# Kernel tuning notes

Hardware: AMD Instinct MI355X
Metric: run time of the kernel (lower is better)

## Reference

```python
import jax, jax.numpy as jnp
import numpy as np

IMG = (3, 64, 64)
CHANNELS = 256
PRIM_DIM = 8
NUM_CLASSES = 50
OUT_DIM = 16
NUM_ROUTING = 3
K = 9
IN_CAPS = (CHANNELS // PRIM_DIM) * 24 * 24  # 18432
DN = ('NCHW', 'OIHW', 'NCHW')


def squash(v, axis=-1):
    sn = jnp.sum(v * v, axis=axis, keepdims=True)
    return sn / (1.0 + sn) * v / (jnp.sqrt(sn) + 1e-8)


def setup_inputs() -> dict:
    key = jax.random.key(0)
    ks = jax.random.split(key, 12)
    s = 0.01
    return {
        'x': jax.random.normal(ks[0], (8,) + IMG, jnp.float32),
        'conv1_w': s * jax.random.normal(ks[1], (CHANNELS, 3, K, K), jnp.float32),
        'conv1_b': jnp.zeros((CHANNELS,), jnp.float32),
        'prim_w': s * jax.random.normal(ks[2], (CHANNELS, CHANNELS, K, K), jnp.float32),
        'prim_b': jnp.zeros((CHANNELS,), jnp.float32),
        'W': s * jax.random.normal(ks[3], (NUM_CLASSES, IN_CAPS, OUT_DIM, PRIM_DIM), jnp.float32),
        'd1_w': s * jax.random.normal(ks[4], (512, OUT_DIM * NUM_CLASSES), jnp.float32),
        'd1_b': jnp.zeros((512,), jnp.float32),
        'd2_w': s * jax.random.normal(ks[5], (1024, 512), jnp.float32),
        'd2_b': jnp.zeros((1024,), jnp.float32),
        'd3_w': s * jax.random.normal(ks[6], (int(np.prod(IMG)), 1024), jnp.float32),
        'd3_b': jnp.zeros((int(np.prod(IMG)),), jnp.float32),
    }


def reference(x, conv1_w, conv1_b, prim_w, prim_b, W, d1_w, d1_b, d2_w, d2_b, d3_w, d3_b):
    B = x.shape[0]
    # conv1 + relu: [B,3,64,64] -> [B,256,56,56]
    h = jax.lax.conv_general_dilated(x, conv1_w, (1, 1), 'VALID', dimension_numbers=DN)
    h = jax.nn.relu(h + conv1_b[None, :, None, None])
    # primary capsules: [B,256,24,24] -> [B,18432,8]
    p = jax.lax.conv_general_dilated(h, prim_w, (2, 2), 'VALID', dimension_numbers=DN)
    p = p + prim_b[None, :, None, None]
    p = p.reshape(B, CHANNELS // PRIM_DIM, p.shape[2], p.shape[3], PRIM_DIM)
    u = squash(p.reshape(B, -1, PRIM_DIM))
    # predictions u_hat: [B, num_caps, in_caps, out_dim]
    u_hat = jnp.einsum('nide,bie->bnid', W, u)
    temp = jax.lax.stop_gradient(u_hat)
    b_log = jnp.zeros((B, NUM_CLASSES, IN_CAPS, 1), jnp.float32)
    for _ in range(NUM_ROUTING - 1):
        sc = jax.nn.softmax(b_log, axis=1)
        v = squash(jnp.sum(sc * temp, axis=2))            # [B,nc,dc]
        b_log = b_log + jnp.einsum('bnid,bnd->bni', temp, v)[..., None]
    sc = jax.nn.softmax(b_log, axis=1)
    v = squash(jnp.sum(sc * u_hat, axis=2))               # [B,nc,dc]
    preds = jnp.linalg.norm(v, axis=-1)                   # [B,nc]
    idx = jnp.argmax(preds, axis=1)
    y = jax.nn.one_hot(idx, NUM_CLASSES, dtype=v.dtype)[..., None]
    r = (v * y).reshape(B, -1)
    r = jax.nn.relu(r @ d1_w.T + d1_b)
    r = jax.nn.relu(r @ d2_w.T + d2_b)
    r = jax.nn.sigmoid(r @ d3_w.T + d3_b)
    recon = r.reshape(B, *IMG)
    return preds, recon
```

## Files before the change

### kernel.cpp

```cpp
#include <hip/hip_runtime.h>

typedef short short8 __attribute__((ext_vector_type(8)));
typedef float f32x4 __attribute__((ext_vector_type(4)));
typedef _Float16 h2 __attribute__((ext_vector_type(2)));

__device__ __forceinline__ unsigned short f2bf(float f) {
  union { float f; unsigned u; } a; a.f = f;
  unsigned r = a.u + 0x7fffu + ((a.u >> 16) & 1u);
  return (unsigned short)(r >> 16);
}

__device__ __forceinline__ h2 u2h2(unsigned w) {
  union { unsigned u; h2 h; } q; q.u = w; return q.h;
}

#if __has_builtin(__builtin_amdgcn_fdot2)
#define FDOT2(a, b, c) __builtin_amdgcn_fdot2((a), (b), (c), false)
#else
#define FDOT2(a, b, c) ((c) + (float)(a)[0] * (float)(b)[0] + (float)(a)[1] * (float)(b)[1])
#endif

__global__ void offtab_k(unsigned* __restrict__ off_tab) {
  const int k = blockIdx.x * 256 + threadIdx.x;
  const int ci = k / 81, rr = k % 81;
  const int ky = rr / 9, kx = rr % 9;
  off_tab[k] = (unsigned)(ci * 3136 + ky * 56 + kx);
}

__global__ __launch_bounds__(256) void wconv_k(const float* __restrict__ pw,
                                               unsigned short* __restrict__ wbf) {
  const int kb = blockIdx.x, co = threadIdx.x;
  const float4* src = (const float4*)(pw + (long)co * 20736 + kb * 8);
  const float4 a = src[0], b = src[1];
  union { unsigned short s[8]; short8 v; } o;
  o.s[0] = f2bf(a.x); o.s[1] = f2bf(a.y); o.s[2] = f2bf(a.z); o.s[3] = f2bf(a.w);
  o.s[4] = f2bf(b.x); o.s[5] = f2bf(b.y); o.s[6] = f2bf(b.z); o.s[7] = f2bf(b.w);
  *reinterpret_cast<short8*>(&wbf[((long)kb * 256 + co) * 8]) = o.v;
}

__global__ __launch_bounds__(256) void conv1_k(const float* __restrict__ x,
                                               const float* __restrict__ w,
                                               const float* __restrict__ bias,
                                               unsigned short* __restrict__ h_bf) {
  __shared__ float xl[12288];
  __shared__ float wl[244];
  const int blk = blockIdx.x;
  const int b = blk >> 8, co = blk & 255;
  const int t = threadIdx.x;
  const float4* xb = (const float4*)(x + b * 12288);
  float4* xl4 = (float4*)xl;
  for (int r = t; r < 3072; r += 256) xl4[r] = xb[r];
  for (int r = t; r < 243; r += 256) wl[r] = w[co * 243 + r];
  __syncthreads();
  if (t >= 224) return;
  const int ox = t % 56, oy0 = (t / 56) * 14;
  float acc[14];
#pragma unroll
  for (int j = 0; j < 14; ++j) acc[j] = 0.f;
  for (int ci = 0; ci < 3; ++ci)
    for (int kx = 0; kx < 9; ++kx) {
      const int base = ci * 4096 + oy0 * 64 + ox + kx;
      float win[22];
#pragma unroll
      for (int q = 0; q < 22; ++q) win[q] = xl[base + q * 64];
#pragma unroll
      for (int ky = 0; ky < 9; ++ky) {
        const float wv = wl[ci * 81 + ky * 9 + kx];
#pragma unroll
        for (int j = 0; j < 14; ++j) acc[j] = fmaf(wv, win[j + ky], acc[j]);
      }
    }
  const float bv = bias[co];
  unsigned short* hp = h_bf + (((long)b * 256 + co) * 56 + oy0) * 56 + ox;
#pragma unroll
  for (int j = 0; j < 14; ++j) {
    float v = acc[j] + bv;
    v = v > 0.f ? v : 0.f;
    hp[j * 56] = f2bf(v);
  }
}

__global__ __launch_bounds__(512) void prim_gemm(const unsigned short* __restrict__ h_bf,
                                                 const uint4* __restrict__ wbf4,
                                                 const unsigned* __restrict__ off_tab,
                                                 float* __restrict__ C_part) {
  __shared__ uint4 A4[256];
  __shared__ uint4 B4[1024];
  const int t = threadIdx.x;
  const int lane = t & 63, w = t >> 6;
  const int mt = blockIdx.x, kz = blockIdx.y;
  const int k0 = kz * 5184;
  const bool isA = (t < 256);
  const int ar = t & 63, ac = (t >> 6) & 3;
  const int m = mt * 64 + ar;
  const int b = m / 576, yx = m % 576;
  const int oy = yx / 24, ox = yx % 24;
  const long base_p = (long)b * 802816 + oy * 112 + ox * 2;
  const int bco = t & 255;
  const int wm = w >> 2, wn = w & 3;
  const int fr = lane & 15, fg = lane >> 4;
  f32x4 acc[2][4];
#pragma unroll
  for (int i2 = 0; i2 < 2; ++i2)
#pragma unroll
    for (int j = 0; j < 4; ++j)
#pragma unroll
      for (int e = 0; e < 4; ++e) acc[i2][j][e] = 0.f;

  union { unsigned short s[8]; uint4 v; } pa;
  uint4 pb0, pb1, pb2, pb3;
  auto loadA = [&](int kt) {
    const int kb = k0 + kt * 32 + ac * 8;
#pragma unroll
    for (int j = 0; j < 8; ++j) pa.s[j] = h_bf[base_p + off_tab[kb + j]];
  };
  auto loadB = [&](int kt) {
    const int kb0 = (k0 + kt * 32) >> 3;
    pb0 = wbf4[(kb0 + 0) * 256 + bco];
    pb1 = wbf4[(kb0 + 1) * 256 + bco];
    pb2 = wbf4[(kb0 + 2) * 256 + bco];
    pb3 = wbf4[(kb0 + 3) * 256 + bco];
  };
  if (isA) loadA(0); else loadB(0);

  const short8* A8 = (const short8*)A4;
  const short8* B8 = (const short8*)B4;
  for (int kt = 0; kt < 162; ++kt) {
    __syncthreads();
    if (isA) {
      A4[ac * 64 + ar] = pa.v;
    } else {
      B4[bco] = pb0;
      B4[256 + bco] = pb1;
      B4[512 + bco] = pb2;
      B4[768 + bco] = pb3;
    }
    if (kt < 161) { if (isA) loadA(kt + 1); else loadB(kt + 1); }
    __syncthreads();
    const short8 a0 = A8[fg * 64 + wm * 32 + fr];
    const short8 a1 = A8[fg * 64 + wm * 32 + 16 + fr];
    const short8 b0 = B8[fg * 256 + wn * 64 + fr];
    const short8 b1 = B8[fg * 256 + wn * 64 + 16 + fr];
    const short8 b2 = B8[fg * 256 + wn * 64 + 32 + fr];
    const short8 b3 = B8[fg * 256 + wn * 64 + 48 + fr];
    acc[0][0] = __builtin_amdgcn_mfma_f32_16x16x32_bf16(a0, b0, acc[0][0], 0, 0, 0);
    acc[0][1] = __builtin_amdgcn_mfma_f32_16x16x32_bf16(a0, b1, acc[0][1], 0, 0, 0);
    acc[0][2] = __builtin_amdgcn_mfma_f32_16x16x32_bf16(a0, b2, acc[0][2], 0, 0, 0);
    acc[0][3] = __builtin_amdgcn_mfma_f32_16x16x32_bf16(a0, b3, acc[0][3], 0, 0, 0);
    acc[1][0] = __builtin_amdgcn_mfma_f32_16x16x32_bf16(a1, b0, acc[1][0], 0, 0, 0);
    acc[1][1] = __builtin_amdgcn_mfma_f32_16x16x32_bf16(a1, b1, acc[1][1], 0, 0, 0);
    acc[1][2] = __builtin_amdgcn_mfma_f32_16x16x32_bf16(a1, b2, acc[1][2], 0, 0, 0);
    acc[1][3] = __builtin_amdgcn_mfma_f32_16x16x32_bf16(a1, b3, acc[1][3], 0, 0, 0);
  }
#pragma unroll
  for (int i2 = 0; i2 < 2; ++i2)
#pragma unroll
    for (int j = 0; j < 4; ++j)
#pragma unroll
      for (int e = 0; e < 4; ++e) {
        const int row = mt * 64 + wm * 32 + i2 * 16 + fg * 4 + e;
        const int col = wn * 64 + j * 16 + fr;
        C_part[((long)kz * 4608 + row) * 256 + col] = acc[i2][j][e];
      }
}

__global__ __launch_bounds__(256) void combine_k(const float* __restrict__ C_part,
                                                 const float* __restrict__ prim_b,
                                                 float* __restrict__ u,
                                                 uint4* __restrict__ u_h) {
  const int cap = blockIdx.x * 256 + threadIdx.x;
  const int b = cap / 18432, r = cap % 18432;
  const int g = r / 576, yx = r % 576;
  const long m = (long)b * 576 + yx;
  float pv[8];
#pragma unroll
  for (int e = 0; e < 8; ++e) pv[e] = prim_b[g * 8 + e];
#pragma unroll
  for (int kz = 0; kz < 4; ++kz) {
    const float4* cp = (const float4*)(C_part + ((long)kz * 4608 + m) * 256 + g * 8);
    const float4 f0 = cp[0], f1 = cp[1];
    pv[0] += f0.x; pv[1] += f0.y; pv[2] += f0.z; pv[3] += f0.w;
    pv[4] += f1.x; pv[5] += f1.y; pv[6] += f1.z; pv[7] += f1.w;
  }
  float sn = 0.f;
#pragma unroll
  for (int e = 0; e < 8; ++e) sn += pv[e] * pv[e];
  const float f = sn / (1.f + sn) / (sqrtf(sn) + 1e-8f);
  float4 o0, o1;
  o0.x = pv[0] * f; o0.y = pv[1] * f; o0.z = pv[2] * f; o0.w = pv[3] * f;
  o1.x = pv[4] * f; o1.y = pv[5] * f; o1.z = pv[6] * f; o1.w = pv[7] * f;
  float4* up = (float4*)(u + (long)cap * 8);
  up[0] = o0; up[1] = o1;
  union { _Float16 h[8]; uint4 v; } oh;
  oh.h[0] = (_Float16)o0.x; oh.h[1] = (_Float16)o0.y; oh.h[2] = (_Float16)o0.z; oh.h[3] = (_Float16)o0.w;
  oh.h[4] = (_Float16)o1.x; oh.h[5] = (_Float16)o1.y; oh.h[6] = (_Float16)o1.z; oh.h[7] = (_Float16)o1.w;
  u_h[cap] = oh.v;
}

__global__ __launch_bounds__(512) void route1_fused(const float* __restrict__ W,
                                                    const float* __restrict__ u,
                                                    uint4* __restrict__ Wh,
                                                    float* __restrict__ S1) {
  __shared__ float4 u_l[8][64];
  __shared__ float red[8][128];
  const int blk = blockIdx.x;
  const int t = threadIdx.x;
  const int i0 = (blk % 576) * 32;
  const long unit = (long)blk * 512 + t;
  {
    const int b = t >> 6, f = t & 63;
    u_l[b][f] = ((const float4*)(u + ((long)b * 18432 + i0) * 8))[f];
  }
  const float4* ws = (const float4*)(W + unit * 8);
  const float4 wa = ws[0], wb = ws[1];
  union { _Float16 h[8]; uint4 v; } o;
  o.h[0] = (_Float16)wa.x; o.h[1] = (_Float16)wa.y; o.h[2] = (_Float16)wa.z; o.h[3] = (_Float16)wa.w;
  o.h[4] = (_Float16)wb.x; o.h[5] = (_Float16)wb.y; o.h[6] = (_Float16)wb.z; o.h[7] = (_Float16)wb.w;
  Wh[unit] = o.v;
  __syncthreads();
  const int il = t >> 4;
  const int w = t >> 6, lane = t & 63;
  float uh[8];
#pragma unroll
  for (int b = 0; b < 8; ++b) {
    const float4 p0 = u_l[b][il * 2], p1 = u_l[b][il * 2 + 1];
    uh[b] = wa.x * p0.x + wa.y * p0.y + wa.z * p0.z + wa.w * p0.w +
            wb.x * p1.x + wb.y * p1.y + wb.z * p1.z + wb.w * p1.w;
  }
#pragma unroll
  for (int b = 0; b < 8; ++b) {
    float v = uh[b];
    v += __shfl_xor(v, 16);
    v += __shfl_xor(v, 32);
    if (lane < 16) red[w][b * 16 + lane] = v;
  }
  __syncthreads();
  if (t < 128) {
    float s = 0.f;
#pragma unroll
    for (int w2 = 0; w2 < 8; ++w2) s += red[w2][t];
    S1[(long)blk * 128 + t] = s;
  }
}

__global__ __launch_bounds__(256) void route_reduce1(const float* __restrict__ S1,
                                                     float* __restrict__ vsum) {
  __shared__ float lds[256];
  const int bn = blockIdx.x;
  const int b = bn / 50, n = bn % 50;
  const int t = threadIdx.x;
  const int kk = t >> 4, dd = t & 15;
  float s = 0.f;
  const float* p = S1 + (long)n * 576 * 128 + b * 16 + dd;
  for (int j = kk; j < 576; j += 16) s += p[(long)j * 128];
  lds[t] = s;
  __syncthreads();
  for (int off = 128; off >= 16; off >>= 1) {
    if (t < off) lds[t] += lds[t + off];
    __syncthreads();
  }
  if (t < 16) {
    const float S = lds[t] * 0.02f;
    float sq = S * S;
    sq += __shfl_xor(sq, 1);
    sq += __shfl_xor(sq, 2);
    sq += __shfl_xor(sq, 4);
    sq += __shfl_xor(sq, 8);
    const float f = sq / (1.f + sq) / (sqrtf(sq) + 1e-8f);
    vsum[bn * 16 + t] += S * f;
  }
}

__global__ __launch_bounds__(256) void route_f16(const uint4* __restrict__ Wb4,
                                                 const uint4* __restrict__ u_h,
                                                 const float* __restrict__ vsum,
                                                 float* __restrict__ S_part) {
  __shared__ uint4 lds4[1600];
  const int t = threadIdx.x;
  const int w = t >> 6, lane = t & 63;
  const int b0 = 2 * w, b1 = 2 * w + 1;
  const bool vn = lane < 50;
  const int nr = vn ? lane : 49;
  const int nxor = nr & 15;
  const int bi = blockIdx.x;
  const int i_base = bi * 16;

  float vs0[16], vs1[16], Sa0[16], Sa1[16];
#pragma unroll
  for (int d = 0; d < 16; ++d) {
    vs0[d] = vsum[(b0 * 50 + nr) * 16 + d];
    vs1[d] = vsum[(b1 * 50 + nr) * 16 + d];
    Sa0[d] = 0.f;
    Sa1[d] = 0.f;
  }

  auto gload = [&](int idx, int i0) -> uint4 {
    const int n = idx >> 5, i2 = (idx >> 4) & 1, c = idx & 15;
    return Wb4[(long)(n * 18432 + i0 + i2) * 16 + c];
  };
  auto lput = [&](int idx, uint4 v) {
    const int n = idx >> 5, i2 = (idx >> 4) & 1, c = idx & 15;
    lds4[n * 32 + i2 * 16 + (c ^ (n & 15))] = v;
  };
  const bool g6 = t < 64;
  uint4 r[7];
  const uint4 zz = make_uint4(0, 0, 0, 0);
#pragma unroll
  for (int k = 0; k < 6; ++k) r[k] = gload(t + 256 * k, i_base);
  r[6] = g6 ? gload(t + 1536, i_base) : zz;

  for (int ch = 0; ch < 8; ++ch) {
    __syncthreads();
#pragma unroll
    for (int k = 0; k < 6; ++k) lput(t + 256 * k, r[k]);
    if (g6) lput(t + 1536, r[6]);
    if (ch < 7) {
      const int ni = i_base + (ch + 1) * 2;
#pragma unroll
      for (int k = 0; k < 6; ++k) r[k] = gload(t + 256 * k, ni);
      if (g6) r[6] = gload(t + 1536, ni);
    }
    __syncthreads();
#pragma unroll
    for (int ii = 0; ii < 2; ++ii) {
      const int i = i_base + ch * 2 + ii;
      const uint4 uv0 = u_h[(long)b0 * 18432 + i];
      const uint4 uv1 = u_h[(long)b1 * 18432 + i];
      const h2 a00 = u2h2(uv0.x), a01 = u2h2(uv0.y), a02 = u2h2(uv0.z), a03 = u2h2(uv0.w);
      const h2 a10 = u2h2(uv1.x), a11 = u2h2(uv1.y), a12 = u2h2(uv1.z), a13 = u2h2(uv1.w);
      const uint4* lrow = &lds4[nr * 32 + ii * 16];
      float uh0[16], uh1[16];
      float lg0 = 0.f, lg1 = 0.f;
#pragma unroll
      for (int d = 0; d < 16; ++d) {
        const uint4 wv = lrow[d ^ nxor];
        const h2 w0 = u2h2(wv.x), w1 = u2h2(wv.y), w2 = u2h2(wv.z), w3 = u2h2(wv.w);
        float s0 = FDOT2(w0, a00, 0.f);
        s0 = FDOT2(w1, a01, s0);
        s0 = FDOT2(w2, a02, s0);
        s0 = FDOT2(w3, a03, s0);
        uh0[d] = s0;
        lg0 = fmaf(s0, vs0[d], lg0);
        float s1 = FDOT2(w0, a10, 0.f);
        s1 = FDOT2(w1, a11, s1);
        s1 = FDOT2(w2, a12, s1);
        s1 = FDOT2(w3, a13, s1);
        uh1[d] = s1;
        lg1 = fmaf(s1, vs1[d], lg1);
      }
      float p0 = vn ? __expf(lg0) : 0.f;
      float p1 = vn ? __expf(lg1) : 0.f;
      float sm0 = p0, sm1 = p1;
      sm0 += __shfl_xor(sm0, 1);
      sm1 += __shfl_xor(sm1, 1);
      sm0 += __shfl_xor(sm0, 2);
      sm1 += __shfl_xor(sm1, 2);
      sm0 += __shfl_xor(sm0, 4);
      sm1 += __shfl_xor(sm1, 4);
      sm0 += __shfl_xor(sm0, 8);
      sm1 += __shfl_xor(sm1, 8);
      sm0 += __shfl_xor(sm0, 16);
      sm1 += __shfl_xor(sm1, 16);
      sm0 += __shfl_xor(sm0, 32);
      sm1 += __shfl_xor(sm1, 32);
      const float sc0 = p0 / sm0;
      const float sc1 = p1 / sm1;
#pragma unroll
      for (int d = 0; d < 16; ++d) {
        Sa0[d] = fmaf(sc0, uh0[d], Sa0[d]);
        Sa1[d] = fmaf(sc1, uh1[d], Sa1[d]);
      }
    }
  }
  if (vn) {
    float* Sp0 = S_part + (long)bi * 6400 + b0 * 800 + lane * 16;
    float* Sp1 = S_part + (long)bi * 6400 + b1 * 800 + lane * 16;
#pragma unroll
    for (int d = 0; d < 16; ++d) {
      Sp0[d] = Sa0[d];
      Sp1[d] = Sa1[d];
    }
  }
}

__global__ __launch_bounds__(512, 4) void route_pass_f32(const float* __restrict__ W,
                                                         const float* __restrict__ u,
                                                         const float* __restrict__ vsum,
                                                         float* __restrict__ S_part) {
  const int t = threadIdx.x;
  const int b = t >> 6;
  const int lane = t & 63;
  const int d = lane & 15, nq = lane >> 4;
  const int qmax = (nq == 3) ? 11 : 13;
  int nn[13];
  float vs[13], Sa[13], uh[13], lg[13];
#pragma unroll
  for (int q = 0; q < 13; ++q) {
    const int n = nq * 13 + q;
    const bool valid = n < 50;
    nn[q] = valid ? n : 49;
    vs[q] = valid ? vsum[(b * 50 + n) * 16 + d] : 0.f;
    Sa[q] = 0.f;
  }
  const int bi = blockIdx.x;
  for (int ii = 0; ii < 32; ++ii) {
    const int i = bi * 32 + ii;
    const float4* up = (const float4*)(u + ((long)b * 18432 + i) * 8);
    const float4 u0 = up[0], u1 = up[1];
    const float* Wi = W + (long)i * 128 + d * 8;
#pragma unroll
    for (int q = 0; q < 13; ++q) {
      const float4* wp = (const float4*)(Wi + (long)nn[q] * 2359296);
      const float4 w0 = wp[0], w1 = wp[1];
      const float s = w0.x * u0.x + w0.y * u0.y + w0.z * u0.z + w0.w * u0.w +
                      w1.x * u1.x + w1.y * u1.y + w1.z * u1.z + w1.w * u1.w;
      uh[q] = s;
      float v = s * vs[q];
      v += __shfl_xor(v, 1);
      v += __shfl_xor(v, 2);
      v += __shfl_xor(v, 4);
      v += __shfl_xor(v, 8);
      lg[q] = (q < qmax) ? v : -1e30f;
    }
    float mx = lg[0];
#pragma unroll
    for (int q = 1; q < 13; ++q) mx = fmaxf(mx, lg[q]);
    mx = fmaxf(mx, __shfl_xor(mx, 16));
    mx = fmaxf(mx, __shfl_xor(mx, 32));
    float sm = 0.f;
#pragma unroll
    for (int q = 0; q < 13; ++q) {
      const float e = __expf(lg[q] - mx);
      lg[q] = e;
      sm += e;
    }
    sm += __shfl_xor(sm, 16);
    sm += __shfl_xor(sm, 32);
    const float inv = 1.f / sm;
#pragma unroll
    for (int q = 0; q < 13; ++q) Sa[q] = fmaf(lg[q] * inv, uh[q], Sa[q]);
  }
  float* Sp = S_part + ((long)bi * 8 + b) * 800;
#pragma unroll
  for (int q = 0; q < 13; ++q)
    if (q < qmax) Sp[(nq * 13 + q) * 16 + d] = Sa[q];
}

__global__ __launch_bounds__(256) void route_reduce(const float* __restrict__ S_part,
                                                    float* __restrict__ vsum,
                                                    float* __restrict__ v3,
                                                    const int pass, const int nparts) {
  __shared__ float lds[256];
  const int bn = blockIdx.x;
  const int b = bn / 50, n = bn % 50;
  const int t = threadIdx.x;
  const int kk = t >> 4, dd = t & 15;
  float s = 0.f;
  const float* p = S_part + (long)b * 800 + n * 16 + dd;
  for (int j = kk; j < nparts; j += 16) s += p[(long)j * 6400];
  lds[t] = s;
  __syncthreads();
  for (int off = 128; off >= 16; off >>= 1) {
    if (t < off) lds[t] += lds[t + off];
    __syncthreads();
  }
  if (t < 16) {
    const float S = lds[t];
    float sq = S * S;
    sq += __shfl_xor(sq, 1);
    sq += __shfl_xor(sq, 2);
    sq += __shfl_xor(sq, 4);
    sq += __shfl_xor(sq, 8);
    const float f = sq / (1.f + sq) / (sqrtf(sq) + 1e-8f);
    const float v = S * f;
    const int o = bn * 16 + t;
    if (pass < 3) vsum[o] += v;
    else v3[o] = v;
  }
}

__global__ __launch_bounds__(512) void head_k(const float* __restrict__ v3,
                                              float* __restrict__ out,
                                              float* __restrict__ selv,
                                              int* __restrict__ idxs) {
  __shared__ float pl[400];
  const int t = threadIdx.x;
  if (t < 400) {
    const float4* vp = (const float4*)(v3 + t * 16);
    const float4 a = vp[0], b = vp[1], c = vp[2], d = vp[3];
    const float s = a.x * a.x + a.y * a.y + a.z * a.z + a.w * a.w +
                    b.x * b.x + b.y * b.y + b.z * b.z + b.w * b.w +
                    c.x * c.x + c.y * c.y + c.z * c.z + c.w * c.w +
                    d.x * d.x + d.y * d.y + d.z * d.z + d.w * d.w;
    const float p = sqrtf(s);
    out[t] = p;
    pl[t] = p;
  }
  __syncthreads();
  if (t < 8) {
    float best = -1e30f;
    int bi = 0;
    for (int n = 0; n < 50; ++n) {
      const float p = pl[t * 50 + n];
      if (p > best) { best = p; bi = n; }
    }
    idxs[t] = bi;
    for (int k = 0; k < 16; ++k) selv[t * 16 + k] = v3[(t * 50 + bi) * 16 + k];
  }
}

__global__ __launch_bounds__(512) void d1_k(const float* __restrict__ selv,
                                            const int* __restrict__ idxs,
                                            const float* __restrict__ d1w,
                                            const float* __restrict__ d1b,
                                            float* __restrict__ r1) {
  const int b = blockIdx.x, j = threadIdx.x;
  const int idx = idxs[b];
  const float* wr = d1w + j * 800 + idx * 16;
  float acc = d1b[j];
#pragma unroll
  for (int k = 0; k < 16; ++k) acc = fmaf(selv[b * 16 + k], wr[k], acc);
  r1[b * 512 + j] = acc > 0.f ? acc : 0.f;
}

__global__ __launch_bounds__(256) void d2_k(const float* __restrict__ r1,
                                            const float* __restrict__ d2w,
                                            const float* __restrict__ d2b,
                                            float* __restrict__ r2) {
  __shared__ float rl[512];
  const int b = blockIdx.y;
  const int j = blockIdx.x * 256 + threadIdx.x;
  for (int r = threadIdx.x; r < 512; r += 256) rl[r] = r1[b * 512 + r];
  __syncthreads();
  const float4* wr = (const float4*)(d2w + (long)j * 512);
  float acc = d2b[j];
  for (int k4 = 0; k4 < 128; ++k4) {
    const float4 w = wr[k4];
    acc += w.x * rl[k4 * 4] + w.y * rl[k4 * 4 + 1] + w.z * rl[k4 * 4 + 2] + w.w * rl[k4 * 4 + 3];
  }
  r2[b * 1024 + j] = acc > 0.f ? acc : 0.f;
}

__global__ __launch_bounds__(256) void d3_k(const float* __restrict__ r2,
                                            const float* __restrict__ d3w,
                                            const float* __restrict__ d3b,
                                            float* __restrict__ out) {
  __shared__ float rl[8192];
  const int j = blockIdx.x * 256 + threadIdx.x;
  float4* rl4 = (float4*)rl;
  for (int r = threadIdx.x; r < 2048; r += 256) rl4[r] = ((const float4*)r2)[r];
  __syncthreads();
  float acc[8];
  const float bv = d3b[j];
#pragma unroll
  for (int b = 0; b < 8; ++b) acc[b] = bv;
  const float4* wr = (const float4*)d3w + (long)j * 256;
  for (int k4 = 0; k4 < 256; ++k4) {
    const float4 w = wr[k4];
#pragma unroll
    for (int b = 0; b < 8; ++b) {
      const int o = b * 1024 + k4 * 4;
      acc[b] += w.x * rl[o] + w.y * rl[o + 1] + w.z * rl[o + 2] + w.w * rl[o + 3];
    }
  }
#pragma unroll
  for (int b = 0; b < 8; ++b)
    out[400 + b * 12288 + j] = 1.f / (1.f + __expf(-acc[b]));
}

extern "C" void kernel_launch(void* const* d_in, const int* in_sizes, int n_in,
                              void* d_out, int out_size, void* d_ws, size_t ws_size,
                              hipStream_t stream) {
  const float* x   = (const float*)d_in[0];
  const float* c1w = (const float*)d_in[1];
  const float* c1b = (const float*)d_in[2];
  const float* pw  = (const float*)d_in[3];
  const float* pb  = (const float*)d_in[4];
  const float* W   = (const float*)d_in[5];
  const float* d1w = (const float*)d_in[6];
  const float* d1b = (const float*)d_in[7];
  const float* d2w = (const float*)d_in[8];
  const float* d2b = (const float*)d_in[9];
  const float* d3w = (const float*)d_in[10];
  const float* d3b = (const float*)d_in[11];
  float* out = (float*)d_out;

  char* wsb = (char*)d_ws;
  size_t off = 0;
  auto alloc = [&](size_t bytes) -> char* {
    char* p = wsb + off;
    off += (bytes + 255) & ~(size_t)255;
    return p;
  };
  unsigned short* h_bf   = (unsigned short*)alloc(12845056);
  unsigned short* wbf    = (unsigned short*)alloc(10616832);
  unsigned*       offt   = (unsigned*)alloc(82944);
  char*           bigA   = alloc(29491200);
  float*          C_part = (float*)bigA;
  float*          S1     = (float*)bigA;
  float*          S_part = (float*)bigA;
  float*          u      = (float*)alloc(4718592);
  uint4*          u_h    = (uint4*)alloc(2359296);
  float*          vsum   = (float*)alloc(25600);
  float*          v3     = (float*)alloc(25600);
  float*          selv   = (float*)alloc(512);
  int*            idxs   = (int*)alloc(64);
  float*          r1     = (float*)alloc(16384);
  float*          r2     = (float*)alloc(32768);
  const size_t off_base = off;
  uint4*          Whf    = (uint4*)alloc(235929600);
  const bool f16_route = (off <= ws_size);
  if (off_base > ws_size) return;

  offtab_k<<<81, 256, 0, stream>>>(offt);
  wconv_k<<<2592, 256, 0, stream>>>(pw, wbf);
  conv1_k<<<2048, 256, 0, stream>>>(x, c1w, c1b, h_bf);
  prim_gemm<<<dim3(72, 4), 512, 0, stream>>>(h_bf, (const uint4*)wbf, offt, C_part);
  combine_k<<<576, 256, 0, stream>>>(C_part, pb, u, u_h);
  hipMemsetAsync(vsum, 0, 25600, stream);
  if (f16_route) {
    route1_fused<<<28800, 512, 0, stream>>>(W, u, Whf, S1);
    route_reduce1<<<400, 256, 0, stream>>>(S1, vsum);
    for (int pass = 2; pass <= 3; ++pass) {
      route_f16<<<1152, 256, 0, stream>>>(Whf, u_h, vsum, S_part);
      route_reduce<<<400, 256, 0, stream>>>(S_part, vsum, v3, pass, 1152);
    }
  } else {
    for (int pass = 1; pass <= 3; ++pass) {
      route_pass_f32<<<576, 512, 0, stream>>>(W, u, vsum, S_part);
      route_reduce<<<400, 256, 0, stream>>>(S_part, vsum, v3, pass, 576);
    }
  }
  head_k<<<1, 512, 0, stream>>>(v3, out, selv, idxs);
  d1_k<<<8, 512, 0, stream>>>(selv, idxs, d1w, d1b, r1);
  d2_k<<<dim3(4, 8), 256, 0, stream>>>(r1, d2w, d2b, r2);
  d3_k<<<48, 256, 0, stream>>>(r2, d3w, d3b, out);
}
```

Measured before the change: 705.1 us.

## Use channel-last activations and tap-major weights; double-buffer LDS in GEMM and routing

The conv1 output is transposed to an NHWC layout by a new kernel, and the primary-capsule weights are reordered tap-major with channel innermost. Each A-tile load in the implicit GEMM then becomes one contiguous 16-byte read instead of eight scattered gathers through an offset table. The prim GEMM and the f16 routing kernel also move to double-buffered LDS, which drops one barrier per iteration and lets the global load for the next tile overlap compute. The cost is an extra transpose pass and twice the LDS per block, which may lower occupancy in route_f16.

```diff
diff --git a/kernel.cpp b/kernel.cpp
--- a/kernel.cpp
+++ b/kernel.cpp
@@ -20,22 +20,13 @@
 #define FDOT2(a, b, c) ((c) + (float)(a)[0] * (float)(b)[0] + (float)(a)[1] * (float)(b)[1])
 #endif
 
-__global__ void offtab_k(unsigned* __restrict__ off_tab) {
-  const int k = blockIdx.x * 256 + threadIdx.x;
-  const int ci = k / 81, rr = k % 81;
-  const int ky = rr / 9, kx = rr % 9;
-  off_tab[k] = (unsigned)(ci * 3136 + ky * 56 + kx);
-}
-
 __global__ __launch_bounds__(256) void wconv_k(const float* __restrict__ pw,
-                                               unsigned short* __restrict__ wbf) {
-  const int kb = blockIdx.x, co = threadIdx.x;
-  const float4* src = (const float4*)(pw + (long)co * 20736 + kb * 8);
-  const float4 a = src[0], b = src[1];
-  union { unsigned short s[8]; short8 v; } o;
-  o.s[0] = f2bf(a.x); o.s[1] = f2bf(a.y); o.s[2] = f2bf(a.z); o.s[3] = f2bf(a.w);
-  o.s[4] = f2bf(b.x); o.s[5] = f2bf(b.y); o.s[6] = f2bf(b.z); o.s[7] = f2bf(b.w);
-  *reinterpret_cast<short8*>(&wbf[((long)kb * 256 + co) * 8]) = o.v;
+                                               unsigned short* __restrict__ pbf) {
+  const int co = blockIdx.x, ci = threadIdx.x;
+  const float* src = pw + (long)co * 20736 + ci * 81;
+  unsigned short* dst = pbf + co * 256 + ci;
+#pragma unroll 9
+  for (int tap = 0; tap < 81; ++tap) dst[(long)tap * 65536] = f2bf(src[tap]);
 }
 
 __global__ __launch_bounds__(256) void conv1_k(const float* __restrict__ x,
@@ -80,12 +71,31 @@
   }
 }
 
-__global__ __launch_bounds__(512) void prim_gemm(const unsigned short* __restrict__ h_bf,
-                                                 const uint4* __restrict__ wbf4,
-                                                 const unsigned* __restrict__ off_tab,
+__global__ __launch_bounds__(256) void ht_k(const unsigned short* __restrict__ h,
+                                            unsigned short* __restrict__ ht) {
+  __shared__ unsigned short lt[56 * 256];
+  const int blk = blockIdx.x;
+  const int b = blk / 56, y = blk % 56;
+  const int t = threadIdx.x;
+  const uint4* src = (const uint4*)(h + (((long)b * 256 + t) * 56 + y) * 56);
+  uint4 v[7];
+#pragma unroll
+  for (int j = 0; j < 7; ++j) v[j] = src[j];
+  const unsigned short* vs = (const unsigned short*)v;
+#pragma unroll
+  for (int xx = 0; xx < 56; ++xx) lt[xx * 256 + t] = vs[xx];
+  __syncthreads();
+  uint4* dst = (uint4*)(ht + ((long)b * 56 + y) * 56 * 256);
+  const uint4* ls = (const uint4*)lt;
+#pragma unroll
+  for (int j = 0; j < 7; ++j) dst[t + 256 * j] = ls[t + 256 * j];
+}
+
+__global__ __launch_bounds__(512) void prim_gemm(const unsigned short* __restrict__ ht,
+                                                 const unsigned short* __restrict__ pbf,
                                                  float* __restrict__ C_part) {
-  __shared__ uint4 A4[256];
-  __shared__ uint4 B4[1024];
+  __shared__ uint4 A4[2][256];
+  __shared__ uint4 B4[2][1024];
   const int t = threadIdx.x;
   const int lane = t & 63, w = t >> 6;
   const int mt = blockIdx.x, kz = blockIdx.y;
@@ -95,7 +105,6 @@
   const int m = mt * 64 + ar;
   const int b = m / 576, yx = m % 576;
   const int oy = yx / 24, ox = yx % 24;
-  const long base_p = (long)b * 802816 + oy * 112 + ox * 2;
   const int bco = t & 255;
   const int wm = w >> 2, wn = w & 3;
   const int fr = lane & 15, fg = lane >> 4;
@@ -107,36 +116,44 @@
 #pragma unroll
       for (int e = 0; e < 4; ++e) acc[i2][j][e] = 0.f;
 
-  union { unsigned short s[8]; uint4 v; } pa;
-  uint4 pb0, pb1, pb2, pb3;
+  uint4 pa, pb0, pb1, pb2, pb3;
   auto loadA = [&](int kt) {
-    const int kb = k0 + kt * 32 + ac * 8;
-#pragma unroll
-    for (int j = 0; j < 8; ++j) pa.s[j] = h_bf[base_p + off_tab[kb + j]];
+    const int k = k0 + kt * 32;
+    const int tap = k >> 8, ci0 = (k & 255) + ac * 8;
+    const int ky = tap / 9, kx = tap % 9;
+    const int iy = 2 * oy + ky, ix = 2 * ox + kx;
+    pa = *(const uint4*)(ht + (((long)b * 56 + iy) * 56 + ix) * 256 + ci0);
   };
   auto loadB = [&](int kt) {
-    const int kb0 = (k0 + kt * 32) >> 3;
-    pb0 = wbf4[(kb0 + 0) * 256 + bco];
-    pb1 = wbf4[(kb0 + 1) * 256 + bco];
-    pb2 = wbf4[(kb0 + 2) * 256 + bco];
-    pb3 = wbf4[(kb0 + 3) * 256 + bco];
+    const int k = k0 + kt * 32;
+    const int tap = k >> 8, ci0 = k & 255;
+    const uint4* s = (const uint4*)(pbf + ((long)tap * 256 + bco) * 256 + ci0);
+    pb0 = s[0]; pb1 = s[1]; pb2 = s[2]; pb3 = s[3];
   };
   if (isA) loadA(0); else loadB(0);
-
-  const short8* A8 = (const short8*)A4;
-  const short8* B8 = (const short8*)B4;
+  if (isA) {
+    A4[0][ac * 64 + ar] = pa;
+  } else {
+    B4[0][bco] = pb0; B4[0][256 + bco] = pb1;
+    B4[0][512 + bco] = pb2; B4[0][768 + bco] = pb3;
+  }
+  if (isA) loadA(1); else loadB(1);
+  __syncthreads();
+
+  int cur = 0;
   for (int kt = 0; kt < 162; ++kt) {
-    __syncthreads();
-    if (isA) {
-      A4[ac * 64 + ar] = pa.v;
-    } else {
-      B4[bco] = pb0;
-      B4[256 + bco] = pb1;
-      B4[512 + bco] = pb2;
-      B4[768 + bco] = pb3;
-    }
-    if (kt < 161) { if (isA) loadA(kt + 1); else loadB(kt + 1); }
-    __syncthreads();
+    const int nxt = cur ^ 1;
+    if (kt < 161) {
+      if (isA) {
+        A4[nxt][ac * 64 + ar] = pa;
+      } else {
+        B4[nxt][bco] = pb0; B4[nxt][256 + bco] = pb1;
+        B4[nxt][512 + bco] = pb2; B4[nxt][768 + bco] = pb3;
+      }
+      if (kt < 160) { if (isA) loadA(kt + 2); else loadB(kt + 2); }
+    }
+    const short8* A8 = (const short8*)A4[cur];
+    const short8* B8 = (const short8*)B4[cur];
     const short8 a0 = A8[fg * 64 + wm * 32 + fr];
     const short8 a1 = A8[fg * 64 + wm * 32 + 16 + fr];
     const short8 b0 = B8[fg * 256 + wn * 64 + fr];
@@ -151,6 +168,8 @@
     acc[1][1] = __builtin_amdgcn_mfma_f32_16x16x32_bf16(a1, b1, acc[1][1], 0, 0, 0);
     acc[1][2] = __builtin_amdgcn_mfma_f32_16x16x32_bf16(a1, b2, acc[1][2], 0, 0, 0);
     acc[1][3] = __builtin_amdgcn_mfma_f32_16x16x32_bf16(a1, b3, acc[1][3], 0, 0, 0);
+    __syncthreads();
+    cur = nxt;
   }
 #pragma unroll
   for (int i2 = 0; i2 < 2; ++i2)
@@ -275,7 +294,7 @@
                                                  const uint4* __restrict__ u_h,
                                                  const float* __restrict__ vsum,
                                                  float* __restrict__ S_part) {
-  __shared__ uint4 lds4[1600];
+  __shared__ uint4 lds4[2][1600];
   const int t = threadIdx.x;
   const int w = t >> 6, lane = t & 63;
   const int b0 = 2 * w, b1 = 2 * w + 1;
@@ -298,9 +317,9 @@
     const int n = idx >> 5, i2 = (idx >> 4) & 1, c = idx & 15;
     return Wb4[(long)(n * 18432 + i0 + i2) * 16 + c];
   };
-  auto lput = [&](int idx, uint4 v) {
+  auto lput = [&](int buf, int idx, uint4 v) {
     const int n = idx >> 5, i2 = (idx >> 4) & 1, c = idx & 15;
-    lds4[n * 32 + i2 * 16 + (c ^ (n & 15))] = v;
+    lds4[buf][n * 32 + i2 * 16 + (c ^ (n & 15))] = v;
   };
   const bool g6 = t < 64;
   uint4 r[7];
@@ -308,19 +327,27 @@
 #pragma unroll
   for (int k = 0; k < 6; ++k) r[k] = gload(t + 256 * k, i_base);
   r[6] = g6 ? gload(t + 1536, i_base) : zz;
+#pragma unroll
+  for (int k = 0; k < 6; ++k) lput(0, t + 256 * k, r[k]);
+  if (g6) lput(0, t + 1536, r[6]);
+#pragma unroll
+  for (int k = 0; k < 6; ++k) r[k] = gload(t + 256 * k, i_base + 2);
+  r[6] = g6 ? gload(t + 1536, i_base + 2) : zz;
+  __syncthreads();
 
   for (int ch = 0; ch < 8; ++ch) {
-    __syncthreads();
-#pragma unroll
-    for (int k = 0; k < 6; ++k) lput(t + 256 * k, r[k]);
-    if (g6) lput(t + 1536, r[6]);
+    const int cur = ch & 1, nbuf = cur ^ 1;
     if (ch < 7) {
-      const int ni = i_base + (ch + 1) * 2;
-#pragma unroll
-      for (int k = 0; k < 6; ++k) r[k] = gload(t + 256 * k, ni);
-      if (g6) r[6] = gload(t + 1536, ni);
-    }
-    __syncthreads();
+#pragma unroll
+      for (int k = 0; k < 6; ++k) lput(nbuf, t + 256 * k, r[k]);
+      if (g6) lput(nbuf, t + 1536, r[6]);
+      if (ch < 6) {
+        const int ni = i_base + (ch + 2) * 2;
+#pragma unroll
+        for (int k = 0; k < 6; ++k) r[k] = gload(t + 256 * k, ni);
+        if (g6) r[6] = gload(t + 1536, ni);
+      }
+    }
 #pragma unroll
     for (int ii = 0; ii < 2; ++ii) {
       const int i = i_base + ch * 2 + ii;
@@ -328,7 +355,7 @@
       const uint4 uv1 = u_h[(long)b1 * 18432 + i];
       const h2 a00 = u2h2(uv0.x), a01 = u2h2(uv0.y), a02 = u2h2(uv0.z), a03 = u2h2(uv0.w);
       const h2 a10 = u2h2(uv1.x), a11 = u2h2(uv1.y), a12 = u2h2(uv1.z), a13 = u2h2(uv1.w);
-      const uint4* lrow = &lds4[nr * 32 + ii * 16];
+      const uint4* lrow = &lds4[cur][nr * 32 + ii * 16];
       float uh0[16], uh1[16];
       float lg0 = 0.f, lg1 = 0.f;
 #pragma unroll
@@ -371,6 +398,7 @@
         Sa1[d] = fmaf(sc1, uh1[d], Sa1[d]);
       }
     }
+    __syncthreads();
   }
   if (vn) {
     float* Sp0 = S_part + (long)bi * 6400 + b0 * 800 + lane * 16;
@@ -593,8 +621,8 @@
     return p;
   };
   unsigned short* h_bf   = (unsigned short*)alloc(12845056);
-  unsigned short* wbf    = (unsigned short*)alloc(10616832);
-  unsigned*       offt   = (unsigned*)alloc(82944);
+  unsigned short* h_t    = (unsigned short*)alloc(12845056);
+  unsigned short* pbf    = (unsigned short*)alloc(10616832);
   char*           bigA   = alloc(29491200);
   float*          C_part = (float*)bigA;
   float*          S1     = (float*)bigA;
@@ -612,10 +640,10 @@
   const bool f16_route = (off <= ws_size);
   if (off_base > ws_size) return;
 
-  offtab_k<<<81, 256, 0, stream>>>(offt);
-  wconv_k<<<2592, 256, 0, stream>>>(pw, wbf);
+  wconv_k<<<256, 256, 0, stream>>>(pw, pbf);
   conv1_k<<<2048, 256, 0, stream>>>(x, c1w, c1b, h_bf);
-  prim_gemm<<<dim3(72, 4), 512, 0, stream>>>(h_bf, (const uint4*)wbf, offt, C_part);
+  ht_k<<<448, 256, 0, stream>>>(h_bf, h_t);
+  prim_gemm<<<dim3(72, 4), 512, 0, stream>>>(h_t, pbf, C_part);
   combine_k<<<576, 256, 0, stream>>>(C_part, pb, u, u_h);
   hipMemsetAsync(vsum, 0, 25600, stream);
   if (f16_route) {
```

Measured after the change: 804.8 us. +14.1%, slower.

## Materialize fp16 u_hat in pass 1 and reuse it in later routing passes

Applied to the files above, without the earlier changes.

The first routing pass now writes the computed prediction vectors u_hat as fp16 in an [n][i][b][d] layout instead of an fp16 copy of W. Passes 2 and 3 read u_hat directly and skip the W·u dot products, the LDS staging and the per-pass u_h loads. The buffer is the same size as the old fp16 W, so HBM traffic per pass stays about the same while compute and synchronisation drop. The trade-off is 2-byte scattered stores in pass 1, which may cost more than the old vectorised W stores.

```diff
diff --git a/kernel.cpp b/kernel.cpp
--- a/kernel.cpp
+++ b/kernel.cpp
@@ -14,11 +14,9 @@
   union { unsigned u; h2 h; } q; q.u = w; return q.h;
 }
 
-#if __has_builtin(__builtin_amdgcn_fdot2)
-#define FDOT2(a, b, c) __builtin_amdgcn_fdot2((a), (b), (c), false)
-#else
-#define FDOT2(a, b, c) ((c) + (float)(a)[0] * (float)(b)[0] + (float)(a)[1] * (float)(b)[1])
-#endif
+__device__ __forceinline__ unsigned short f2h(float f) {
+  union { _Float16 h; unsigned short s; } q; q.h = (_Float16)f; return q.s;
+}
 
 __global__ void offtab_k(unsigned* __restrict__ off_tab) {
   const int k = blockIdx.x * 256 + threadIdx.x;
@@ -166,8 +164,7 @@
 
 __global__ __launch_bounds__(256) void combine_k(const float* __restrict__ C_part,
                                                  const float* __restrict__ prim_b,
-                                                 float* __restrict__ u,
-                                                 uint4* __restrict__ u_h) {
+                                                 float* __restrict__ u) {
   const int cap = blockIdx.x * 256 + threadIdx.x;
   const int b = cap / 18432, r = cap % 18432;
   const int g = r / 576, yx = r % 576;
@@ -191,20 +188,17 @@
   o1.x = pv[4] * f; o1.y = pv[5] * f; o1.z = pv[6] * f; o1.w = pv[7] * f;
   float4* up = (float4*)(u + (long)cap * 8);
   up[0] = o0; up[1] = o1;
-  union { _Float16 h[8]; uint4 v; } oh;
-  oh.h[0] = (_Float16)o0.x; oh.h[1] = (_Float16)o0.y; oh.h[2] = (_Float16)o0.z; oh.h[3] = (_Float16)o0.w;
-  oh.h[4] = (_Float16)o1.x; oh.h[5] = (_Float16)o1.y; oh.h[6] = (_Float16)o1.z; oh.h[7] = (_Float16)o1.w;
-  u_h[cap] = oh.v;
 }
 
 __global__ __launch_bounds__(512) void route1_fused(const float* __restrict__ W,
                                                     const float* __restrict__ u,
-                                                    uint4* __restrict__ Wh,
+                                                    unsigned short* __restrict__ uhat,
                                                     float* __restrict__ S1) {
   __shared__ float4 u_l[8][64];
   __shared__ float red[8][128];
   const int blk = blockIdx.x;
   const int t = threadIdx.x;
+  const int n = blk / 576;
   const int i0 = (blk % 576) * 32;
   const long unit = (long)blk * 512 + t;
   {
@@ -213,12 +207,8 @@
   }
   const float4* ws = (const float4*)(W + unit * 8);
   const float4 wa = ws[0], wb = ws[1];
-  union { _Float16 h[8]; uint4 v; } o;
-  o.h[0] = (_Float16)wa.x; o.h[1] = (_Float16)wa.y; o.h[2] = (_Float16)wa.z; o.h[3] = (_Float16)wa.w;
-  o.h[4] = (_Float16)wb.x; o.h[5] = (_Float16)wb.y; o.h[6] = (_Float16)wb.z; o.h[7] = (_Float16)wb.w;
-  Wh[unit] = o.v;
-  __syncthreads();
-  const int il = t >> 4;
+  __syncthreads();
+  const int il = t >> 4, d = t & 15;
   const int w = t >> 6, lane = t & 63;
   float uh[8];
 #pragma unroll
@@ -227,6 +217,9 @@
     uh[b] = wa.x * p0.x + wa.y * p0.y + wa.z * p0.z + wa.w * p0.w +
             wb.x * p1.x + wb.y * p1.y + wb.z * p1.z + wb.w * p1.w;
   }
+  unsigned short* up = uhat + ((long)n * 18432 + i0 + il) * 128 + d;
+#pragma unroll
+  for (int b = 0; b < 8; ++b) up[b * 16] = f2h(uh[b]);
 #pragma unroll
   for (int b = 0; b < 8; ++b) {
     float v = uh[b];
@@ -271,17 +264,14 @@
   }
 }
 
-__global__ __launch_bounds__(256) void route_f16(const uint4* __restrict__ Wb4,
-                                                 const uint4* __restrict__ u_h,
-                                                 const float* __restrict__ vsum,
-                                                 float* __restrict__ S_part) {
-  __shared__ uint4 lds4[1600];
+__global__ __launch_bounds__(256) void route_uhat(const uint4* __restrict__ uh4,
+                                                  const float* __restrict__ vsum,
+                                                  float* __restrict__ S_part) {
   const int t = threadIdx.x;
   const int w = t >> 6, lane = t & 63;
-  const int b0 = 2 * w, b1 = 2 * w + 1;
+  const int b0 = 2 * w;
   const bool vn = lane < 50;
   const int nr = vn ? lane : 49;
-  const int nxor = nr & 15;
   const int bi = blockIdx.x;
   const int i_base = bi * 16;
 
@@ -289,92 +279,85 @@
 #pragma unroll
   for (int d = 0; d < 16; ++d) {
     vs0[d] = vsum[(b0 * 50 + nr) * 16 + d];
-    vs1[d] = vsum[(b1 * 50 + nr) * 16 + d];
+    vs1[d] = vsum[((b0 + 1) * 50 + nr) * 16 + d];
     Sa0[d] = 0.f;
     Sa1[d] = 0.f;
   }
 
-  auto gload = [&](int idx, int i0) -> uint4 {
-    const int n = idx >> 5, i2 = (idx >> 4) & 1, c = idx & 15;
-    return Wb4[(long)(n * 18432 + i0 + i2) * 16 + c];
+  auto base4 = [&](int i) -> long {
+    return ((long)nr * 18432 + i) * 16 + b0 * 2;
   };
-  auto lput = [&](int idx, uint4 v) {
-    const int n = idx >> 5, i2 = (idx >> 4) & 1, c = idx & 15;
-    lds4[n * 32 + i2 * 16 + (c ^ (n & 15))] = v;
-  };
-  const bool g6 = t < 64;
-  uint4 r[7];
-  const uint4 zz = make_uint4(0, 0, 0, 0);
-#pragma unroll
-  for (int k = 0; k < 6; ++k) r[k] = gload(t + 256 * k, i_base);
-  r[6] = g6 ? gload(t + 1536, i_base) : zz;
-
-  for (int ch = 0; ch < 8; ++ch) {
-    __syncthreads();
-#pragma unroll
-    for (int k = 0; k < 6; ++k) lput(t + 256 * k, r[k]);
-    if (g6) lput(t + 1536, r[6]);
-    if (ch < 7) {
-      const int ni = i_base + (ch + 1) * 2;
-#pragma unroll
-      for (int k = 0; k < 6; ++k) r[k] = gload(t + 256 * k, ni);
-      if (g6) r[6] = gload(t + 1536, ni);
-    }
-    __syncthreads();
-#pragma unroll
-    for (int ii = 0; ii < 2; ++ii) {
-      const int i = i_base + ch * 2 + ii;
-      const uint4 uv0 = u_h[(long)b0 * 18432 + i];
-      const uint4 uv1 = u_h[(long)b1 * 18432 + i];
-      const h2 a00 = u2h2(uv0.x), a01 = u2h2(uv0.y), a02 = u2h2(uv0.z), a03 = u2h2(uv0.w);
-      const h2 a10 = u2h2(uv1.x), a11 = u2h2(uv1.y), a12 = u2h2(uv1.z), a13 = u2h2(uv1.w);
-      const uint4* lrow = &lds4[nr * 32 + ii * 16];
-      float uh0[16], uh1[16];
-      float lg0 = 0.f, lg1 = 0.f;
-#pragma unroll
-      for (int d = 0; d < 16; ++d) {
-        const uint4 wv = lrow[d ^ nxor];
-        const h2 w0 = u2h2(wv.x), w1 = u2h2(wv.y), w2 = u2h2(wv.z), w3 = u2h2(wv.w);
-        float s0 = FDOT2(w0, a00, 0.f);
-        s0 = FDOT2(w1, a01, s0);
-        s0 = FDOT2(w2, a02, s0);
-        s0 = FDOT2(w3, a03, s0);
-        uh0[d] = s0;
-        lg0 = fmaf(s0, vs0[d], lg0);
-        float s1 = FDOT2(w0, a10, 0.f);
-        s1 = FDOT2(w1, a11, s1);
-        s1 = FDOT2(w2, a12, s1);
-        s1 = FDOT2(w3, a13, s1);
-        uh1[d] = s1;
-        lg1 = fmaf(s1, vs1[d], lg1);
+  uint4 c0, c1, c2, c3;
+  {
+    const long p = base4(i_base);
+    c0 = uh4[p]; c1 = uh4[p + 1]; c2 = uh4[p + 2]; c3 = uh4[p + 3];
+  }
+  for (int ii = 0; ii < 16; ++ii) {
+    uint4 n0, n1, n2, n3;
+    if (ii < 15) {
+      const long p = base4(i_base + ii + 1);
+      n0 = uh4[p]; n1 = uh4[p + 1]; n2 = uh4[p + 2]; n3 = uh4[p + 3];
+    }
+    float uh0[16], uh1[16];
+    {
+      const unsigned* w0 = (const unsigned*)&c0;
+#pragma unroll
+      for (int q = 0; q < 4; ++q) {
+        const h2 hh = u2h2(w0[q]);
+        uh0[q * 2] = (float)hh[0]; uh0[q * 2 + 1] = (float)hh[1];
       }
-      float p0 = vn ? __expf(lg0) : 0.f;
-      float p1 = vn ? __expf(lg1) : 0.f;
-      float sm0 = p0, sm1 = p1;
-      sm0 += __shfl_xor(sm0, 1);
-      sm1 += __shfl_xor(sm1, 1);
-      sm0 += __shfl_xor(sm0, 2);
-      sm1 += __shfl_xor(sm1, 2);
-      sm0 += __shfl_xor(sm0, 4);
-      sm1 += __shfl_xor(sm1, 4);
-      sm0 += __shfl_xor(sm0, 8);
-      sm1 += __shfl_xor(sm1, 8);
-      sm0 += __shfl_xor(sm0, 16);
-      sm1 += __shfl_xor(sm1, 16);
-      sm0 += __shfl_xor(sm0, 32);
-      sm1 += __shfl_xor(sm1, 32);
-      const float sc0 = p0 / sm0;
-      const float sc1 = p1 / sm1;
-#pragma unroll
-      for (int d = 0; d < 16; ++d) {
-        Sa0[d] = fmaf(sc0, uh0[d], Sa0[d]);
-        Sa1[d] = fmaf(sc1, uh1[d], Sa1[d]);
+      const unsigned* w1 = (const unsigned*)&c1;
+#pragma unroll
+      for (int q = 0; q < 4; ++q) {
+        const h2 hh = u2h2(w1[q]);
+        uh0[8 + q * 2] = (float)hh[0]; uh0[8 + q * 2 + 1] = (float)hh[1];
       }
-    }
+      const unsigned* w2 = (const unsigned*)&c2;
+#pragma unroll
+      for (int q = 0; q < 4; ++q) {
+        const h2 hh = u2h2(w2[q]);
+        uh1[q * 2] = (float)hh[0]; uh1[q * 2 + 1] = (float)hh[1];
+      }
+      const unsigned* w3 = (const unsigned*)&c3;
+#pragma unroll
+      for (int q = 0; q < 4; ++q) {
+        const h2 hh = u2h2(w3[q]);
+        uh1[8 + q * 2] = (float)hh[0]; uh1[8 + q * 2 + 1] = (float)hh[1];
+      }
+    }
+    float lg0 = 0.f, lg1 = 0.f;
+#pragma unroll
+    for (int d = 0; d < 16; ++d) {
+      lg0 = fmaf(uh0[d], vs0[d], lg0);
+      lg1 = fmaf(uh1[d], vs1[d], lg1);
+    }
+    float p0 = vn ? __expf(lg0) : 0.f;
+    float p1 = vn ? __expf(lg1) : 0.f;
+    float sm0 = p0, sm1 = p1;
+    sm0 += __shfl_xor(sm0, 1);
+    sm1 += __shfl_xor(sm1, 1);
+    sm0 += __shfl_xor(sm0, 2);
+    sm1 += __shfl_xor(sm1, 2);
+    sm0 += __shfl_xor(sm0, 4);
+    sm1 += __shfl_xor(sm1, 4);
+    sm0 += __shfl_xor(sm0, 8);
+    sm1 += __shfl_xor(sm1, 8);
+    sm0 += __shfl_xor(sm0, 16);
+    sm1 += __shfl_xor(sm1, 16);
+    sm0 += __shfl_xor(sm0, 32);
+    sm1 += __shfl_xor(sm1, 32);
+    const float sc0 = p0 / sm0;
+    const float sc1 = p1 / sm1;
+#pragma unroll
+    for (int d = 0; d < 16; ++d) {
+      Sa0[d] = fmaf(sc0, uh0[d], Sa0[d]);
+      Sa1[d] = fmaf(sc1, uh1[d], Sa1[d]);
+    }
+    c0 = n0; c1 = n1; c2 = n2; c3 = n3;
   }
   if (vn) {
     float* Sp0 = S_part + (long)bi * 6400 + b0 * 800 + lane * 16;
-    float* Sp1 = S_part + (long)bi * 6400 + b1 * 800 + lane * 16;
+    float* Sp1 = Sp0 + 800;
 #pragma unroll
     for (int d = 0; d < 16; ++d) {
       Sp0[d] = Sa0[d];
@@ -600,7 +583,6 @@
   float*          S1     = (float*)bigA;
   float*          S_part = (float*)bigA;
   float*          u      = (float*)alloc(4718592);
-  uint4*          u_h    = (uint4*)alloc(2359296);
   float*          vsum   = (float*)alloc(25600);
   float*          v3     = (float*)alloc(25600);
   float*          selv   = (float*)alloc(512);
@@ -608,21 +590,21 @@
   float*          r1     = (float*)alloc(16384);
   float*          r2     = (float*)alloc(32768);
   const size_t off_base = off;
-  uint4*          Whf    = (uint4*)alloc(235929600);
-  const bool f16_route = (off <= ws_size);
+  unsigned short* uhat   = (unsigned short*)alloc(235929600);
+  const bool uhat_route = (off <= ws_size);
   if (off_base > ws_size) return;
 
   offtab_k<<<81, 256, 0, stream>>>(offt);
   wconv_k<<<2592, 256, 0, stream>>>(pw, wbf);
   conv1_k<<<2048, 256, 0, stream>>>(x, c1w, c1b, h_bf);
   prim_gemm<<<dim3(72, 4), 512, 0, stream>>>(h_bf, (const uint4*)wbf, offt, C_part);
-  combine_k<<<576, 256, 0, stream>>>(C_part, pb, u, u_h);
+  combine_k<<<576, 256, 0, stream>>>(C_part, pb, u);
   hipMemsetAsync(vsum, 0, 25600, stream);
-  if (f16_route) {
-    route1_fused<<<28800, 512, 0, stream>>>(W, u, Whf, S1);
+  if (uhat_route) {
+    route1_fused<<<28800, 512, 0, stream>>>(W, u, uhat, S1);
     route_reduce1<<<400, 256, 0, stream>>>(S1, vsum);
     for (int pass = 2; pass <= 3; ++pass) {
-      route_f16<<<1152, 256, 0, stream>>>(Whf, u_h, vsum, S_part);
+      route_uhat<<<1152, 256, 0, stream>>>((const uint4*)uhat, vsum, S_part);
       route_reduce<<<400, 256, 0, stream>>>(S_part, vsum, v3, pass, 1152);
     }
   } else {
```

New measurement: 708.6 us. About the same (+0.5%).
